# Optimization experiments

Hardware: AMD Instinct MI355X
Metric: run time of the kernel (lower is better)

The kernel has to match this reference:

```python
import jax, jax.numpy as jnp
import numpy as np

B, T, D, H = 2, 2048, 768, 12
HS = D // H           # head_size = 64
FF = 4 * D            # feed_forward_multiplier = 4 -> hidden 3072
HALF = FF // 2        # SwiGLU halves hidden -> 1536
EPS = 1e-8


def rmsnorm(x, scale):
    # RMSNorm with p=-1: full-dim L2 norm / sqrt(d), then x/(rms+eps)*scale
    d = x.shape[-1]
    rms = jnp.linalg.norm(x, axis=-1, keepdims=True) * (d ** -0.5)
    return scale * (x / (rms + EPS))


def setup_inputs() -> dict:
    key = jax.random.key(0)
    ks = jax.random.split(key, 12)
    s = 0.02
    return {
        "x":  jax.random.normal(ks[0], (B, T, D), dtype=jnp.float32),
        "Wq": jax.random.normal(ks[1], (H, D, HS), dtype=jnp.float32) * s,
        "Wk": jax.random.normal(ks[2], (H, D, HS), dtype=jnp.float32) * s,
        "Wv": jax.random.normal(ks[3], (H, D, HS), dtype=jnp.float32) * s,
        "Wo": jax.random.normal(ks[4], (D, D), dtype=jnp.float32) * s,
        "bo": jnp.zeros((D,), dtype=jnp.float32),
        "W1": jax.random.normal(ks[5], (D, FF), dtype=jnp.float32) * s,
        "b1": jnp.zeros((FF,), dtype=jnp.float32),
        "W2": jax.random.normal(ks[6], (HALF, D), dtype=jnp.float32) * s,
        "b2": jnp.zeros((D,), dtype=jnp.float32),
        "g1": jnp.ones((D,), dtype=jnp.float32),
        "g2": jnp.ones((D,), dtype=jnp.float32),
    }


def reference(x, Wq, Wk, Wv, Wo, bo, W1, b1, W2, b2, g1, g2):
    Bx, Tx, Dx = x.shape
    # --- Multi-head causal attention (pre-RMSNorm, residual) ---
    h = rmsnorm(x, g1)
    q = jnp.einsum('btd,hdk->bhtk', h, Wq)
    k = jnp.einsum('btd,hdk->bhtk', h, Wk)
    v = jnp.einsum('btd,hdk->bhtk', h, Wv)
    # NOTE: original scales by C**-0.5 where C = embed_dim (not head_size)
    scores = jnp.einsum('bhtk,bhsk->bhts', q, k) * (Dx ** -0.5)
    causal = jnp.tril(jnp.ones((Tx, Tx), dtype=bool))
    scores = jnp.where(causal, scores, -jnp.inf)
    wei = jax.nn.softmax(scores, axis=-1)
    attn = jnp.einsum('bhts,bhsk->bhtk', wei, v)
    attn = attn.transpose(0, 2, 1, 3).reshape(Bx, Tx, Dx)  # concat heads
    x = x + attn @ Wo + bo
    # --- SwiGLU FFN (pre-RMSNorm, residual) ---
    h2 = rmsnorm(x, g2)
    u = h2 @ W1 + b1
    a, gate = jnp.split(u, 2, axis=-1)  # chunk: first half = value, second = gate
    x = x + (jax.nn.silu(gate) * a) @ W2 + b2
    return x
```

## Files before the change

kernel.cpp:

```cpp
#include <hip/hip_runtime.h>
#include <math.h>

#define TDIM 2048
#define DDIM 768
#define NH   12
#define NROWS 4096
#define EPSV 1e-8f
#define SCALE 0.03608439182435161f

typedef __bf16 bf16_t;
typedef bf16_t bf16x8 __attribute__((ext_vector_type(8)));
typedef bf16_t bf16x4 __attribute__((ext_vector_type(4)));
typedef float  floatx4 __attribute__((ext_vector_type(4)));

__device__ __forceinline__ void glds16(const bf16_t* g, bf16_t* l) {
    __builtin_amdgcn_global_load_lds(
        (const __attribute__((address_space(1))) void*)g,
        (__attribute__((address_space(3))) void*)l, 16, 0, 0);
}

__global__ __launch_bounds__(256) void pack_all(
    const float* __restrict__ Wq, const float* __restrict__ Wk,
    const float* __restrict__ Wv, const float* __restrict__ Wo,
    const float* __restrict__ W1, const float* __restrict__ W2,
    bf16_t* __restrict__ qkvw, bf16_t* __restrict__ wo,
    bf16_t* __restrict__ w1, bf16_t* __restrict__ w2)
{
    int bid = blockIdx.x;
    const float* src; bf16_t* dst;
    int srcld, dstld, k0, n0;
    if (bid < 144) {
        int kx = bid % 12, nx = bid / 12;
        src = Wo; dst = wo; srcld = 768; dstld = 768; k0 = kx * 64; n0 = nx * 64;
    } else if (bid < 720) {
        int t = bid - 144; int kx = t % 12, nx = t / 12;
        src = W1; dst = w1; srcld = 3072; dstld = 768; k0 = kx * 64; n0 = nx * 64;
    } else if (bid < 1008) {
        int t = bid - 720; int kx = t % 24, nx = t / 24;
        src = W2; dst = w2; srcld = 768; dstld = 1536; k0 = kx * 64; n0 = nx * 64;
    } else {
        int t = bid - 1008; int kx = t % 12, y = t / 12;
        int sel = y / 12, h = y - sel * 12;
        src = ((sel == 0) ? Wq : (sel == 1) ? Wk : Wv) + (size_t)h * 768 * 64;
        dst = qkvw + (size_t)(sel * 768 + h * 64) * 768;
        srcld = 64; dstld = 768; k0 = kx * 64; n0 = 0;
    }
    __shared__ float Ts[64][65];
    int tid = threadIdx.x;
    int r = tid >> 2, c = (tid & 3) * 16;
    const float* s = src + (size_t)(k0 + r) * srcld + n0 + c;
    #pragma unroll
    for (int i = 0; i < 4; i++) {
        float4 t = *(const float4*)(s + i * 4);
        Ts[r][c + i*4 + 0] = t.x; Ts[r][c + i*4 + 1] = t.y;
        Ts[r][c + i*4 + 2] = t.z; Ts[r][c + i*4 + 3] = t.w;
    }
    __syncthreads();
    int n = tid >> 2, kk = (tid & 3) * 16;
    bf16x8 o0, o1;
    #pragma unroll
    for (int i = 0; i < 8; i++) {
        o0[i] = (bf16_t)Ts[kk + i][n];
        o1[i] = (bf16_t)Ts[kk + 8 + i][n];
    }
    bf16_t* d = dst + (size_t)(n0 + n) * dstld + k0 + kk;
    *(bf16x8*)d = o0;
    *(bf16x8*)(d + 8) = o1;
}

__global__ __launch_bounds__(256) void rmsnorm_bf(
    const float* __restrict__ x, const float* __restrict__ g,
    bf16_t* __restrict__ out)
{
    int row = blockIdx.x;
    int tid = threadIdx.x;
    const float* xr = x + (size_t)row * DDIM;
    float v0 = xr[tid], v1 = xr[tid + 256], v2 = xr[tid + 512];
    float s = v0*v0 + v1*v1 + v2*v2;
    #pragma unroll
    for (int off = 32; off > 0; off >>= 1)
        s += __shfl_down(s, off, 64);
    __shared__ float red[4];
    __shared__ float tot;
    if ((tid & 63) == 0) red[tid >> 6] = s;
    __syncthreads();
    if (tid == 0) tot = red[0] + red[1] + red[2] + red[3];
    __syncthreads();
    float rms = sqrtf(tot * (1.0f / DDIM));
    float inv = 1.0f / (rms + EPSV);
    bf16_t* orow = out + (size_t)row * DDIM;
    orow[tid]       = (bf16_t)(g[tid]       * v0 * inv);
    orow[tid + 256] = (bf16_t)(g[tid + 256] * v1 * inv);
    orow[tid + 512] = (bf16_t)(g[tid + 512] * v2 * inv);
}

template<int TM>
__global__ __launch_bounds__(256) void gemm_bf16(
    const bf16_t* __restrict__ A, const bf16_t* __restrict__ BT, int K,
    float* __restrict__ Cf, bf16_t* __restrict__ Cb, int ldc,
    const float* __restrict__ bias, const float* __restrict__ resid)
{
    constexpr int MT = TM / 32;
    __shared__ bf16_t As[2][TM][32];
    __shared__ bf16_t Bs[2][128][32];
    int tid = threadIdx.x;
    int wave = tid >> 6, lane = tid & 63;
    int lrow = lane & 15, quad = lane >> 4;
    int wm = wave >> 1, wn = wave & 1;

    int m0 = blockIdx.y * TM;
    int n0 = blockIdx.x * 128;

    int srow = lane >> 2, scol = (lane & 3) * 8;
    const bf16_t* Ag = A  + ((size_t)m0 + wave * (TM/4) + srow) * K + scol;
    const bf16_t* Bg = BT + ((size_t)n0 + wave * 32 + srow) * K + scol;

    #pragma unroll
    for (int i = 0; i < TM/64; i++)
        glds16(Ag + (size_t)(i*16) * K, &As[0][wave*(TM/4) + i*16][0]);
    #pragma unroll
    for (int i = 0; i < 2; i++)
        glds16(Bg + (size_t)(i*16) * K, &Bs[0][wave*32 + i*16][0]);

    floatx4 acc[MT][4];
    #pragma unroll
    for (int mt = 0; mt < MT; mt++)
        #pragma unroll
        for (int nt = 0; nt < 4; nt++)
            #pragma unroll
            for (int r = 0; r < 4; r++) acc[mt][nt][r] = 0.f;

    int nit = K / 32;
    for (int it = 0; it < nit; it++) {
        __syncthreads();
        if (it + 1 < nit) {
            int nb = (it + 1) & 1, ko = (it + 1) * 32;
            #pragma unroll
            for (int i = 0; i < TM/64; i++)
                glds16(Ag + (size_t)(i*16) * K + ko, &As[nb][wave*(TM/4) + i*16][0]);
            #pragma unroll
            for (int i = 0; i < 2; i++)
                glds16(Bg + (size_t)(i*16) * K + ko, &Bs[nb][wave*32 + i*16][0]);
        }
        int cb = it & 1;
        bf16x8 af[MT], bfr[4];
        #pragma unroll
        for (int mt = 0; mt < MT; mt++)
            af[mt] = *(const bf16x8*)&As[cb][wm*(TM/2) + mt*16 + lrow][quad * 8];
        #pragma unroll
        for (int nt = 0; nt < 4; nt++)
            bfr[nt] = *(const bf16x8*)&Bs[cb][wn*64 + nt*16 + lrow][quad * 8];
        #pragma unroll
        for (int mt = 0; mt < MT; mt++)
            #pragma unroll
            for (int nt = 0; nt < 4; nt++)
                acc[mt][nt] = __builtin_amdgcn_mfma_f32_16x16x32_bf16(
                    bfr[nt], af[mt], acc[mt][nt], 0, 0, 0);
    }

    int crow0 = m0 + wm * (TM/2);
    int ccol0 = n0 + wn * 64;
    #pragma unroll
    for (int mt = 0; mt < MT; mt++) {
        int row = crow0 + mt * 16 + lrow;
        #pragma unroll
        for (int nt = 0; nt < 4; nt++) {
            int col = ccol0 + nt * 16 + quad * 4;
            size_t off = (size_t)row * ldc + col;
            float4 bv = make_float4(0.f, 0.f, 0.f, 0.f);
            if (bias) bv = *(const float4*)(bias + col);
            float4 rs = make_float4(0.f, 0.f, 0.f, 0.f);
            if (resid) rs = *(const float4*)(resid + off);
            floatx4 a = acc[mt][nt];
            if (Cf) {
                float4 v;
                v.x = a[0] + bv.x + rs.x; v.y = a[1] + bv.y + rs.y;
                v.z = a[2] + bv.z + rs.z; v.w = a[3] + bv.w + rs.w;
                *(float4*)(Cf + off) = v;
            } else {
                bf16x4 v;
                v[0] = (bf16_t)(a[0] + bv.x + rs.x);
                v[1] = (bf16_t)(a[1] + bv.y + rs.y);
                v[2] = (bf16_t)(a[2] + bv.z + rs.z);
                v[3] = (bf16_t)(a[3] + bv.w + rs.w);
                *(bf16x4*)(Cb + off) = v;
            }
        }
    }
}

__global__ __launch_bounds__(256) void gemm_v(
    const bf16_t* __restrict__ A, const bf16_t* __restrict__ BT,
    bf16_t* __restrict__ vt)
{
    const int K = 768;
    __shared__ bf16_t As[2][128][32];
    __shared__ bf16_t Bs[2][128][32];
    int tid = threadIdx.x;
    int wave = tid >> 6, lane = tid & 63;
    int lrow = lane & 15, quad = lane >> 4;
    int wm = wave >> 1, wn = wave & 1;

    int m0 = blockIdx.y * 128;
    int n0 = blockIdx.x * 128;

    int srow = lane >> 2, scol = (lane & 3) * 8;
    const bf16_t* Ag = A  + ((size_t)m0 + wave * 32 + srow) * K + scol;
    const bf16_t* Bg = BT + ((size_t)n0 + wave * 32 + srow) * K + scol;

    #pragma unroll
    for (int i = 0; i < 2; i++) {
        glds16(Ag + (size_t)(i*16) * K, &As[0][wave*32 + i*16][0]);
        glds16(Bg + (size_t)(i*16) * K, &Bs[0][wave*32 + i*16][0]);
    }

    floatx4 acc[4][4];
    #pragma unroll
    for (int mt = 0; mt < 4; mt++)
        #pragma unroll
        for (int nt = 0; nt < 4; nt++)
            #pragma unroll
            for (int r = 0; r < 4; r++) acc[mt][nt][r] = 0.f;

    int nit = K / 32;
    for (int it = 0; it < nit; it++) {
        __syncthreads();
        if (it + 1 < nit) {
            int nb = (it + 1) & 1, ko = (it + 1) * 32;
            #pragma unroll
            for (int i = 0; i < 2; i++) {
                glds16(Ag + (size_t)(i*16) * K + ko, &As[nb][wave*32 + i*16][0]);
                glds16(Bg + (size_t)(i*16) * K + ko, &Bs[nb][wave*32 + i*16][0]);
            }
        }
        int cb = it & 1;
        bf16x8 af[4], bfr[4];
        #pragma unroll
        for (int mt = 0; mt < 4; mt++)
            af[mt] = *(const bf16x8*)&As[cb][wm*64 + mt*16 + lrow][quad * 8];
        #pragma unroll
        for (int nt = 0; nt < 4; nt++)
            bfr[nt] = *(const bf16x8*)&Bs[cb][wn*64 + nt*16 + lrow][quad * 8];
        #pragma unroll
        for (int mt = 0; mt < 4; mt++)
            #pragma unroll
            for (int nt = 0; nt < 4; nt++)
                acc[mt][nt] = __builtin_amdgcn_mfma_f32_16x16x32_bf16(
                    af[mt], bfr[nt], acc[mt][nt], 0, 0, 0);
    }

    #pragma unroll
    for (int nt = 0; nt < 4; nt++) {
        int d = n0 + wn * 64 + nt * 16 + lrow;
        int h = d >> 6, dl = d & 63;
        #pragma unroll
        for (int mt = 0; mt < 4; mt++) {
            int mg = m0 + wm * 64 + mt * 16 + quad * 4;
            int b = mg >> 11, tl = mg & 2047;
            bf16x4 v;
            #pragma unroll
            for (int r = 0; r < 4; r++) v[r] = (bf16_t)acc[mt][nt][r];
            *(bf16x4*)(vt + (((size_t)(b * NH + h) * 64 + dl) * TDIM + tl)) = v;
        }
    }
}

__global__ __launch_bounds__(256) void gemm_ffn1(
    const bf16_t* __restrict__ A, const bf16_t* __restrict__ W1t,
    const float* __restrict__ b1, bf16_t* __restrict__ sw)
{
    const int K = 768;
    __shared__ bf16_t As[2][64][32];
    __shared__ bf16_t Ba[2][128][32];
    __shared__ bf16_t Bg[2][128][32];
    int tid = threadIdx.x;
    int wave = tid >> 6, lane = tid & 63;
    int lrow = lane & 15, quad = lane >> 4;
    int wm = wave >> 1, wn = wave & 1;

    int m0 = blockIdx.y * 64;
    int n0 = blockIdx.x * 128;

    int srow = lane >> 2, scol = (lane & 3) * 8;
    const bf16_t* Agp = A   + ((size_t)m0 + wave * 16 + srow) * K + scol;
    const bf16_t* Bap = W1t + ((size_t)n0 + wave * 32 + srow) * K + scol;
    const bf16_t* Bgp = W1t + ((size_t)(1536 + n0) + wave * 32 + srow) * K + scol;

    glds16(Agp, &As[0][wave*16][0]);
    #pragma unroll
    for (int i = 0; i < 2; i++) {
        glds16(Bap + (size_t)(i*16) * K, &Ba[0][wave*32 + i*16][0]);
        glds16(Bgp + (size_t)(i*16) * K, &Bg[0][wave*32 + i*16][0]);
    }

    floatx4 acc_a[2][4], acc_g[2][4];
    #pragma unroll
    for (int mt = 0; mt < 2; mt++)
        #pragma unroll
        for (int nt = 0; nt < 4; nt++)
            #pragma unroll
            for (int r = 0; r < 4; r++) { acc_a[mt][nt][r] = 0.f; acc_g[mt][nt][r] = 0.f; }

    int nit = K / 32;
    for (int it = 0; it < nit; it++) {
        __syncthreads();
        if (it + 1 < nit) {
            int nb = (it + 1) & 1, ko = (it + 1) * 32;
            glds16(Agp + ko, &As[nb][wave*16][0]);
            #pragma unroll
            for (int i = 0; i < 2; i++) {
                glds16(Bap + (size_t)(i*16) * K + ko, &Ba[nb][wave*32 + i*16][0]);
                glds16(Bgp + (size_t)(i*16) * K + ko, &Bg[nb][wave*32 + i*16][0]);
            }
        }
        int cb = it & 1;
        bf16x8 af[2], ba[4], bg[4];
        #pragma unroll
        for (int mt = 0; mt < 2; mt++)
            af[mt] = *(const bf16x8*)&As[cb][wm*32 + mt*16 + lrow][quad * 8];
        #pragma unroll
        for (int nt = 0; nt < 4; nt++) {
            ba[nt] = *(const bf16x8*)&Ba[cb][wn*64 + nt*16 + lrow][quad * 8];
            bg[nt] = *(const bf16x8*)&Bg[cb][wn*64 + nt*16 + lrow][quad * 8];
        }
        #pragma unroll
        for (int mt = 0; mt < 2; mt++)
            #pragma unroll
            for (int nt = 0; nt < 4; nt++) {
                acc_a[mt][nt] = __builtin_amdgcn_mfma_f32_16x16x32_bf16(
                    ba[nt], af[mt], acc_a[mt][nt], 0, 0, 0);
                acc_g[mt][nt] = __builtin_amdgcn_mfma_f32_16x16x32_bf16(
                    bg[nt], af[mt], acc_g[mt][nt], 0, 0, 0);
            }
    }

    #pragma unroll
    for (int mt = 0; mt < 2; mt++) {
        int row = m0 + wm * 32 + mt * 16 + lrow;
        #pragma unroll
        for (int nt = 0; nt < 4; nt++) {
            int col = n0 + wn * 64 + nt * 16 + quad * 4;
            float4 bva = *(const float4*)(b1 + col);
            float4 bvg = *(const float4*)(b1 + 1536 + col);
            float av[4] = { acc_a[mt][nt][0] + bva.x, acc_a[mt][nt][1] + bva.y,
                            acc_a[mt][nt][2] + bva.z, acc_a[mt][nt][3] + bva.w };
            float gv[4] = { acc_g[mt][nt][0] + bvg.x, acc_g[mt][nt][1] + bvg.y,
                            acc_g[mt][nt][2] + bvg.z, acc_g[mt][nt][3] + bvg.w };
            bf16x4 v;
            #pragma unroll
            for (int r = 0; r < 4; r++)
                v[r] = (bf16_t)(av[r] * (gv[r] / (1.0f + __expf(-gv[r]))));
            *(bf16x4*)(sw + (size_t)row * 1536 + col) = v;
        }
    }
}

__global__ __launch_bounds__(256) void attn_mfma(
    const bf16_t* __restrict__ qk, const bf16_t* __restrict__ vt,
    bf16_t* __restrict__ o)
{
    const int QS = 1536;
    int bid = blockIdx.x;
    int j = bid & 255, slot = bid >> 8;
    int qt, bh;
    if (slot == 0)      { qt = j & 31;        bh = j >> 5; }
    else if (slot == 1) { qt = 31 - (j & 31); bh = 8 + (j >> 5); }
    else                { qt = j >> 3;        bh = 16 + (j & 7); }
    int b = bh / NH, h = bh - b * NH;
    int tid = threadIdx.x;
    int wave = tid >> 6, lane = tid & 63;
    int lrow = lane & 15, quad = lane >> 4;

    __shared__ bf16_t Ks[64][72];
    __shared__ bf16_t Vt[64][72];
    __shared__ bf16_t Ps[4][16][72];

    size_t rbase = (size_t)b * TDIM;
    int q0 = qt * 64, qrow_w = q0 + wave * 16;

    const bf16_t* qp = qk + (rbase + qrow_w + lrow) * QS + h * 64;
    bf16x8 qf[2];
    qf[0] = *(const bf16x8*)(qp + quad * 8);
    qf[1] = *(const bf16x8*)(qp + 32 + quad * 8);

    floatx4 o_acc[4];
    #pragma unroll
    for (int mt = 0; mt < 4; mt++)
        #pragma unroll
        for (int r = 0; r < 4; r++) o_acc[mt][r] = 0.f;
    float m_r = -INFINITY, l_r = 0.f;

    int srow = tid >> 2;
    int scol = (tid & 3) * 16;

    for (int s = 0; s <= qt; s++) {
        __syncthreads();
        {
            const bf16_t* kp = qk + (rbase + s * 64 + srow) * QS + 768 + h * 64 + scol;
            *(bf16x8*)&Ks[srow][scol]     = *(const bf16x8*)kp;
            *(bf16x8*)&Ks[srow][scol + 8] = *(const bf16x8*)(kp + 8);
            const bf16_t* vp = vt + ((size_t)bh * 64 + srow) * TDIM + s * 64 + scol;
            *(bf16x8*)&Vt[srow][scol]     = *(const bf16x8*)vp;
            *(bf16x8*)&Vt[srow][scol + 8] = *(const bf16x8*)(vp + 8);
        }
        __syncthreads();

        floatx4 sfrag[4];
        #pragma unroll
        for (int nt = 0; nt < 4; nt++) {
            floatx4 a;
            #pragma unroll
            for (int r = 0; r < 4; r++) a[r] = 0.f;
            #pragma unroll
            for (int kf = 0; kf < 2; kf++) {
                bf16x8 afr = *(const bf16x8*)&Ks[nt * 16 + lrow][kf * 32 + quad * 8];
                a = __builtin_amdgcn_mfma_f32_16x16x32_bf16(afr, qf[kf], a, 0, 0, 0);
            }
            sfrag[nt] = a;
        }

        if (s == qt) {
            int qg = qrow_w + lrow;
            #pragma unroll
            for (int nt = 0; nt < 4; nt++)
                #pragma unroll
                for (int r = 0; r < 4; r++) {
                    int kc = s * 64 + nt * 16 + quad * 4 + r;
                    sfrag[nt][r] = (kc > qg) ? -INFINITY : sfrag[nt][r] * SCALE;
                }
        } else {
            #pragma unroll
            for (int nt = 0; nt < 4; nt++)
                #pragma unroll
                for (int r = 0; r < 4; r++) sfrag[nt][r] *= SCALE;
        }

        float mx = sfrag[0][0];
        #pragma unroll
        for (int nt = 0; nt < 4; nt++)
            #pragma unroll
            for (int r = 0; r < 4; r++) mx = fmaxf(mx, sfrag[nt][r]);
        mx = fmaxf(mx, __shfl_xor(mx, 16, 64));
        mx = fmaxf(mx, __shfl_xor(mx, 32, 64));
        float mn = fmaxf(m_r, mx);
        float alpha = __expf(m_r - mn);
        m_r = mn;

        float ls = 0.f;
        #pragma unroll
        for (int nt = 0; nt < 4; nt++) {
            bf16x4 pv;
            #pragma unroll
            for (int r = 0; r < 4; r++) {
                float p = __expf(sfrag[nt][r] - mn);
                ls += p;
                pv[r] = (bf16_t)p;
            }
            *(bf16x4*)&Ps[wave][lrow][nt * 16 + quad * 4] = pv;
        }
        ls += __shfl_xor(ls, 16, 64);
        ls += __shfl_xor(ls, 32, 64);
        l_r = l_r * alpha + ls;
        #pragma unroll
        for (int mt = 0; mt < 4; mt++)
            #pragma unroll
            for (int r = 0; r < 4; r++) o_acc[mt][r] *= alpha;

        #pragma unroll
        for (int kf = 0; kf < 2; kf++) {
            bf16x8 pfr = *(const bf16x8*)&Ps[wave][lrow][kf * 32 + quad * 8];
            #pragma unroll
            for (int mt = 0; mt < 4; mt++) {
                bf16x8 vfr = *(const bf16x8*)&Vt[mt * 16 + lrow][kf * 32 + quad * 8];
                o_acc[mt] = __builtin_amdgcn_mfma_f32_16x16x32_bf16(vfr, pfr, o_acc[mt], 0, 0, 0);
            }
        }
    }

    float inv = 1.0f / l_r;
    size_t rb = (rbase + qrow_w + lrow) * DDIM + h * 64;
    #pragma unroll
    for (int mt = 0; mt < 4; mt++) {
        bf16x4 ov;
        #pragma unroll
        for (int r = 0; r < 4; r++) ov[r] = (bf16_t)(o_acc[mt][r] * inv);
        *(bf16x4*)(o + rb + mt * 16 + quad * 4) = ov;
    }
}

extern "C" void kernel_launch(void* const* d_in, const int* in_sizes, int n_in,
                              void* d_out, int out_size, void* d_ws, size_t ws_size,
                              hipStream_t stream) {
    const float* x  = (const float*)d_in[0];
    const float* Wq = (const float*)d_in[1];
    const float* Wk = (const float*)d_in[2];
    const float* Wv = (const float*)d_in[3];
    const float* Wo = (const float*)d_in[4];
    const float* bo = (const float*)d_in[5];
    const float* W1 = (const float*)d_in[6];
    const float* b1 = (const float*)d_in[7];
    const float* W2 = (const float*)d_in[8];
    const float* b2 = (const float*)d_in[9];
    const float* g1 = (const float*)d_in[10];
    const float* g2 = (const float*)d_in[11];
    float* out = (float*)d_out;
    char* ws = (char*)d_ws;

    bf16_t* qkvw_bt = (bf16_t*)(ws);
    bf16_t* wo_bt   = (bf16_t*)(ws + 3538944);
    bf16_t* w1_bt   = (bf16_t*)(ws + 4718592);
    bf16_t* w2_bt   = (bf16_t*)(ws + 9437184);
    bf16_t* h_bf    = (bf16_t*)(ws + 11796480);
    bf16_t* qk      = (bf16_t*)(ws + 18087936);
    bf16_t* attn_bf = (bf16_t*)(ws + 30670848);
    bf16_t* sw_bf   = (bf16_t*)(ws + 36962304);
    bf16_t* vt      = (bf16_t*)(ws + 49545216);

    pack_all<<<1440, 256, 0, stream>>>(Wq, Wk, Wv, Wo, W1, W2,
                                       qkvw_bt, wo_bt, w1_bt, w2_bt);

    rmsnorm_bf<<<NROWS, 256, 0, stream>>>(x, g1, h_bf);

    gemm_bf16<128><<<dim3(12, 32), 256, 0, stream>>>(
        h_bf, qkvw_bt, 768, nullptr, qk, 1536, nullptr, nullptr);

    gemm_v<<<dim3(6, 32), 256, 0, stream>>>(h_bf, qkvw_bt + (size_t)1536 * 768, vt);

    attn_mfma<<<768, 256, 0, stream>>>(qk, vt, attn_bf);

    gemm_bf16<64><<<dim3(6, 64), 256, 0, stream>>>(
        attn_bf, wo_bt, 768, out, nullptr, 768, bo, x);

    rmsnorm_bf<<<NROWS, 256, 0, stream>>>(out, g2, h_bf);

    gemm_ffn1<<<dim3(12, 64), 256, 0, stream>>>(h_bf, w1_bt, b1, sw_bf);

    gemm_bf16<64><<<dim3(6, 64), 256, 0, stream>>>(
        sw_bf, w2_bt, 1536, out, nullptr, 768, b2, out);
}
```

Before: 287.6 us.

## Fold attention scale into Wq and switch GEMMs to K=64 single-buffer steps

The softmax scale is multiplied into the Q weights when they are packed, so the attention kernel no longer scales every score. All three GEMM kernels swap their double-buffered K=32 prefetch pipeline for a synchronous loop that loads a K=64 slice into two halves and waits on a barrier before computing. This halves the number of loop iterations and barriers per tile but drops the overlap of global loads with MFMA work. Rounding Wq to bf16 after scaling changes numerics slightly.

```diff
diff --git a/kernel.cpp b/kernel.cpp
--- a/kernel.cpp
+++ b/kernel.cpp
@@ -29,6 +29,7 @@
     int bid = blockIdx.x;
     const float* src; bf16_t* dst;
     int srcld, dstld, k0, n0;
+    float mult = 1.0f;
     if (bid < 144) {
         int kx = bid % 12, nx = bid / 12;
         src = Wo; dst = wo; srcld = 768; dstld = 768; k0 = kx * 64; n0 = nx * 64;
@@ -44,6 +45,7 @@
         src = ((sel == 0) ? Wq : (sel == 1) ? Wk : Wv) + (size_t)h * 768 * 64;
         dst = qkvw + (size_t)(sel * 768 + h * 64) * 768;
         srcld = 64; dstld = 768; k0 = kx * 64; n0 = 0;
+        if (sel == 0) mult = SCALE;
     }
     __shared__ float Ts[64][65];
     int tid = threadIdx.x;
@@ -60,8 +62,8 @@
     bf16x8 o0, o1;
     #pragma unroll
     for (int i = 0; i < 8; i++) {
-        o0[i] = (bf16_t)Ts[kk + i][n];
-        o1[i] = (bf16_t)Ts[kk + 8 + i][n];
+        o0[i] = (bf16_t)(Ts[kk + i][n] * mult);
+        o1[i] = (bf16_t)(Ts[kk + 8 + i][n] * mult);
     }
     bf16_t* d = dst + (size_t)(n0 + n) * dstld + k0 + kk;
     *(bf16x8*)d = o0;
@@ -101,8 +103,8 @@
     const float* __restrict__ bias, const float* __restrict__ resid)
 {
     constexpr int MT = TM / 32;
-    __shared__ bf16_t As[2][TM][32];
-    __shared__ bf16_t Bs[2][128][32];
+    __shared__ bf16_t As0[TM][32], As1[TM][32];
+    __shared__ bf16_t Bs0[128][32], Bs1[128][32];
     int tid = threadIdx.x;
     int wave = tid >> 6, lane = tid & 63;
     int lrow = lane & 15, quad = lane >> 4;
@@ -115,13 +117,6 @@
     const bf16_t* Ag = A  + ((size_t)m0 + wave * (TM/4) + srow) * K + scol;
     const bf16_t* Bg = BT + ((size_t)n0 + wave * 32 + srow) * K + scol;
 
-    #pragma unroll
-    for (int i = 0; i < TM/64; i++)
-        glds16(Ag + (size_t)(i*16) * K, &As[0][wave*(TM/4) + i*16][0]);
-    #pragma unroll
-    for (int i = 0; i < 2; i++)
-        glds16(Bg + (size_t)(i*16) * K, &Bs[0][wave*32 + i*16][0]);
-
     floatx4 acc[MT][4];
     #pragma unroll
     for (int mt = 0; mt < MT; mt++)
@@ -130,32 +125,40 @@
             #pragma unroll
             for (int r = 0; r < 4; r++) acc[mt][nt][r] = 0.f;
 
-    int nit = K / 32;
-    for (int it = 0; it < nit; it++) {
-        __syncthreads();
-        if (it + 1 < nit) {
-            int nb = (it + 1) & 1, ko = (it + 1) * 32;
-            #pragma unroll
-            for (int i = 0; i < TM/64; i++)
-                glds16(Ag + (size_t)(i*16) * K + ko, &As[nb][wave*(TM/4) + i*16][0]);
-            #pragma unroll
-            for (int i = 0; i < 2; i++)
-                glds16(Bg + (size_t)(i*16) * K + ko, &Bs[nb][wave*32 + i*16][0]);
-        }
-        int cb = it & 1;
-        bf16x8 af[MT], bfr[4];
+    for (int k0 = 0; k0 < K; k0 += 64) {
+        __syncthreads();
+        #pragma unroll
+        for (int i = 0; i < TM/64; i++) {
+            glds16(Ag + (size_t)(i*16) * K + k0,      &As0[wave*(TM/4) + i*16][0]);
+            glds16(Ag + (size_t)(i*16) * K + k0 + 32, &As1[wave*(TM/4) + i*16][0]);
+        }
+        #pragma unroll
+        for (int i = 0; i < 2; i++) {
+            glds16(Bg + (size_t)(i*16) * K + k0,      &Bs0[wave*32 + i*16][0]);
+            glds16(Bg + (size_t)(i*16) * K + k0 + 32, &Bs1[wave*32 + i*16][0]);
+        }
+        __syncthreads();
+
+        bf16x8 af0[MT], af1[MT], bf0[4], bf1[4];
+        #pragma unroll
+        for (int mt = 0; mt < MT; mt++) {
+            af0[mt] = *(const bf16x8*)&As0[wm*(TM/2) + mt*16 + lrow][quad * 8];
+            af1[mt] = *(const bf16x8*)&As1[wm*(TM/2) + mt*16 + lrow][quad * 8];
+        }
+        #pragma unroll
+        for (int nt = 0; nt < 4; nt++) {
+            bf0[nt] = *(const bf16x8*)&Bs0[wn*64 + nt*16 + lrow][quad * 8];
+            bf1[nt] = *(const bf16x8*)&Bs1[wn*64 + nt*16 + lrow][quad * 8];
+        }
         #pragma unroll
         for (int mt = 0; mt < MT; mt++)
-            af[mt] = *(const bf16x8*)&As[cb][wm*(TM/2) + mt*16 + lrow][quad * 8];
-        #pragma unroll
-        for (int nt = 0; nt < 4; nt++)
-            bfr[nt] = *(const bf16x8*)&Bs[cb][wn*64 + nt*16 + lrow][quad * 8];
-        #pragma unroll
-        for (int mt = 0; mt < MT; mt++)
-            #pragma unroll
-            for (int nt = 0; nt < 4; nt++)
+            #pragma unroll
+            for (int nt = 0; nt < 4; nt++) {
                 acc[mt][nt] = __builtin_amdgcn_mfma_f32_16x16x32_bf16(
-                    bfr[nt], af[mt], acc[mt][nt], 0, 0, 0);
+                    bf0[nt], af0[mt], acc[mt][nt], 0, 0, 0);
+                acc[mt][nt] = __builtin_amdgcn_mfma_f32_16x16x32_bf16(
+                    bf1[nt], af1[mt], acc[mt][nt], 0, 0, 0);
+            }
     }
 
     int crow0 = m0 + wm * (TM/2);
@@ -194,8 +197,8 @@
     bf16_t* __restrict__ vt)
 {
     const int K = 768;
-    __shared__ bf16_t As[2][128][32];
-    __shared__ bf16_t Bs[2][128][32];
+    __shared__ bf16_t As0[128][32], As1[128][32];
+    __shared__ bf16_t Bs0[128][32], Bs1[128][32];
     int tid = threadIdx.x;
     int wave = tid >> 6, lane = tid & 63;
     int lrow = lane & 15, quad = lane >> 4;
@@ -208,12 +211,6 @@
     const bf16_t* Ag = A  + ((size_t)m0 + wave * 32 + srow) * K + scol;
     const bf16_t* Bg = BT + ((size_t)n0 + wave * 32 + srow) * K + scol;
 
-    #pragma unroll
-    for (int i = 0; i < 2; i++) {
-        glds16(Ag + (size_t)(i*16) * K, &As[0][wave*32 + i*16][0]);
-        glds16(Bg + (size_t)(i*16) * K, &Bs[0][wave*32 + i*16][0]);
-    }
-
     floatx4 acc[4][4];
     #pragma unroll
     for (int mt = 0; mt < 4; mt++)
@@ -222,31 +219,37 @@
             #pragma unroll
             for (int r = 0; r < 4; r++) acc[mt][nt][r] = 0.f;
 
-    int nit = K / 32;
-    for (int it = 0; it < nit; it++) {
-        __syncthreads();
-        if (it + 1 < nit) {
-            int nb = (it + 1) & 1, ko = (it + 1) * 32;
-            #pragma unroll
-            for (int i = 0; i < 2; i++) {
-                glds16(Ag + (size_t)(i*16) * K + ko, &As[nb][wave*32 + i*16][0]);
-                glds16(Bg + (size_t)(i*16) * K + ko, &Bs[nb][wave*32 + i*16][0]);
-            }
-        }
-        int cb = it & 1;
-        bf16x8 af[4], bfr[4];
+    for (int k0 = 0; k0 < K; k0 += 64) {
+        __syncthreads();
+        #pragma unroll
+        for (int i = 0; i < 2; i++) {
+            glds16(Ag + (size_t)(i*16) * K + k0,      &As0[wave*32 + i*16][0]);
+            glds16(Ag + (size_t)(i*16) * K + k0 + 32, &As1[wave*32 + i*16][0]);
+            glds16(Bg + (size_t)(i*16) * K + k0,      &Bs0[wave*32 + i*16][0]);
+            glds16(Bg + (size_t)(i*16) * K + k0 + 32, &Bs1[wave*32 + i*16][0]);
+        }
+        __syncthreads();
+
+        bf16x8 af0[4], af1[4], bf0[4], bf1[4];
+        #pragma unroll
+        for (int mt = 0; mt < 4; mt++) {
+            af0[mt] = *(const bf16x8*)&As0[wm*64 + mt*16 + lrow][quad * 8];
+            af1[mt] = *(const bf16x8*)&As1[wm*64 + mt*16 + lrow][quad * 8];
+        }
+        #pragma unroll
+        for (int nt = 0; nt < 4; nt++) {
+            bf0[nt] = *(const bf16x8*)&Bs0[wn*64 + nt*16 + lrow][quad * 8];
+            bf1[nt] = *(const bf16x8*)&Bs1[wn*64 + nt*16 + lrow][quad * 8];
+        }
         #pragma unroll
         for (int mt = 0; mt < 4; mt++)
-            af[mt] = *(const bf16x8*)&As[cb][wm*64 + mt*16 + lrow][quad * 8];
-        #pragma unroll
-        for (int nt = 0; nt < 4; nt++)
-            bfr[nt] = *(const bf16x8*)&Bs[cb][wn*64 + nt*16 + lrow][quad * 8];
-        #pragma unroll
-        for (int mt = 0; mt < 4; mt++)
-            #pragma unroll
-            for (int nt = 0; nt < 4; nt++)
+            #pragma unroll
+            for (int nt = 0; nt < 4; nt++) {
                 acc[mt][nt] = __builtin_amdgcn_mfma_f32_16x16x32_bf16(
-                    af[mt], bfr[nt], acc[mt][nt], 0, 0, 0);
+                    af0[mt], bf0[nt], acc[mt][nt], 0, 0, 0);
+                acc[mt][nt] = __builtin_amdgcn_mfma_f32_16x16x32_bf16(
+                    af1[mt], bf1[nt], acc[mt][nt], 0, 0, 0);
+            }
     }
 
     #pragma unroll
@@ -270,9 +273,9 @@
     const float* __restrict__ b1, bf16_t* __restrict__ sw)
 {
     const int K = 768;
-    __shared__ bf16_t As[2][64][32];
-    __shared__ bf16_t Ba[2][128][32];
-    __shared__ bf16_t Bg[2][128][32];
+    __shared__ bf16_t As0[64][32], As1[64][32];
+    __shared__ bf16_t Ba0[128][32], Ba1[128][32];
+    __shared__ bf16_t Bg0[128][32], Bg1[128][32];
     int tid = threadIdx.x;
     int wave = tid >> 6, lane = tid & 63;
     int lrow = lane & 15, quad = lane >> 4;
@@ -286,13 +289,6 @@
     const bf16_t* Bap = W1t + ((size_t)n0 + wave * 32 + srow) * K + scol;
     const bf16_t* Bgp = W1t + ((size_t)(1536 + n0) + wave * 32 + srow) * K + scol;
 
-    glds16(Agp, &As[0][wave*16][0]);
-    #pragma unroll
-    for (int i = 0; i < 2; i++) {
-        glds16(Bap + (size_t)(i*16) * K, &Ba[0][wave*32 + i*16][0]);
-        glds16(Bgp + (size_t)(i*16) * K, &Bg[0][wave*32 + i*16][0]);
-    }
-
     floatx4 acc_a[2][4], acc_g[2][4];
     #pragma unroll
     for (int mt = 0; mt < 2; mt++)
@@ -301,36 +297,44 @@
             #pragma unroll
             for (int r = 0; r < 4; r++) { acc_a[mt][nt][r] = 0.f; acc_g[mt][nt][r] = 0.f; }
 
-    int nit = K / 32;
-    for (int it = 0; it < nit; it++) {
-        __syncthreads();
-        if (it + 1 < nit) {
-            int nb = (it + 1) & 1, ko = (it + 1) * 32;
-            glds16(Agp + ko, &As[nb][wave*16][0]);
-            #pragma unroll
-            for (int i = 0; i < 2; i++) {
-                glds16(Bap + (size_t)(i*16) * K + ko, &Ba[nb][wave*32 + i*16][0]);
-                glds16(Bgp + (size_t)(i*16) * K + ko, &Bg[nb][wave*32 + i*16][0]);
-            }
-        }
-        int cb = it & 1;
-        bf16x8 af[2], ba[4], bg[4];
-        #pragma unroll
-        for (int mt = 0; mt < 2; mt++)
-            af[mt] = *(const bf16x8*)&As[cb][wm*32 + mt*16 + lrow][quad * 8];
-        #pragma unroll
-        for (int nt = 0; nt < 4; nt++) {
-            ba[nt] = *(const bf16x8*)&Ba[cb][wn*64 + nt*16 + lrow][quad * 8];
-            bg[nt] = *(const bf16x8*)&Bg[cb][wn*64 + nt*16 + lrow][quad * 8];
+    for (int k0 = 0; k0 < K; k0 += 64) {
+        __syncthreads();
+        glds16(Agp + k0,      &As0[wave*16][0]);
+        glds16(Agp + k0 + 32, &As1[wave*16][0]);
+        #pragma unroll
+        for (int i = 0; i < 2; i++) {
+            glds16(Bap + (size_t)(i*16) * K + k0,      &Ba0[wave*32 + i*16][0]);
+            glds16(Bap + (size_t)(i*16) * K + k0 + 32, &Ba1[wave*32 + i*16][0]);
+            glds16(Bgp + (size_t)(i*16) * K + k0,      &Bg0[wave*32 + i*16][0]);
+            glds16(Bgp + (size_t)(i*16) * K + k0 + 32, &Bg1[wave*32 + i*16][0]);
+        }
+        __syncthreads();
+
+        bf16x8 af0[2], af1[2], ba0[4], ba1[4], bg0[4], bg1[4];
+        #pragma unroll
+        for (int mt = 0; mt < 2; mt++) {
+            af0[mt] = *(const bf16x8*)&As0[wm*32 + mt*16 + lrow][quad * 8];
+            af1[mt] = *(const bf16x8*)&As1[wm*32 + mt*16 + lrow][quad * 8];
+        }
+        #pragma unroll
+        for (int nt = 0; nt < 4; nt++) {
+            ba0[nt] = *(const bf16x8*)&Ba0[wn*64 + nt*16 + lrow][quad * 8];
+            ba1[nt] = *(const bf16x8*)&Ba1[wn*64 + nt*16 + lrow][quad * 8];
+            bg0[nt] = *(const bf16x8*)&Bg0[wn*64 + nt*16 + lrow][quad * 8];
+            bg1[nt] = *(const bf16x8*)&Bg1[wn*64 + nt*16 + lrow][quad * 8];
         }
         #pragma unroll
         for (int mt = 0; mt < 2; mt++)
             #pragma unroll
             for (int nt = 0; nt < 4; nt++) {
                 acc_a[mt][nt] = __builtin_amdgcn_mfma_f32_16x16x32_bf16(
-                    ba[nt], af[mt], acc_a[mt][nt], 0, 0, 0);
+                    ba0[nt], af0[mt], acc_a[mt][nt], 0, 0, 0);
+                acc_a[mt][nt] = __builtin_amdgcn_mfma_f32_16x16x32_bf16(
+                    ba1[nt], af1[mt], acc_a[mt][nt], 0, 0, 0);
                 acc_g[mt][nt] = __builtin_amdgcn_mfma_f32_16x16x32_bf16(
-                    bg[nt], af[mt], acc_g[mt][nt], 0, 0, 0);
+                    bg0[nt], af0[mt], acc_g[mt][nt], 0, 0, 0);
+                acc_g[mt][nt] = __builtin_amdgcn_mfma_f32_16x16x32_bf16(
+                    bg1[nt], af1[mt], acc_g[mt][nt], 0, 0, 0);
             }
     }
 
@@ -426,13 +430,8 @@
                 #pragma unroll
                 for (int r = 0; r < 4; r++) {
                     int kc = s * 64 + nt * 16 + quad * 4 + r;
-                    sfrag[nt][r] = (kc > qg) ? -INFINITY : sfrag[nt][r] * SCALE;
+                    if (kc > qg) sfrag[nt][r] = -INFINITY;
                 }
-        } else {
-            #pragma unroll
-            for (int nt = 0; nt < 4; nt++)
-                #pragma unroll
-                for (int r = 0; r < 4; r++) sfrag[nt][r] *= SCALE;
         }
 
         float mx = sfrag[0][0];
```

Measured after the change: 283.7 us. Within noise of the previous version (-1.3%).
